# Performance work log

Hardware: AMD Instinct MI355X
Metric: run time of the kernel (lower is better)

The kernel has to match this reference:

```python
import jax, jax.numpy as jnp
import numpy as np

DEGREE = 4
NUM_CHARTS = 8
N = 16384
IN_DIM = 29  # 3*(2*4+1) + 2 procedural params


def positional_encoding(x, degree=DEGREE):
    # Faithful to torch order: [x, sin(2^1 pi x), cos(2^1 pi x), ..., sin(2^d pi x), cos(2^d pi x)]
    pe = [x]
    for d in range(1, degree + 1):
        s = (2.0 ** d) * np.pi
        pe.append(jnp.sin(s * x))
        pe.append(jnp.cos(s * x))
    return jnp.concatenate(pe, axis=-1)


def setup_inputs() -> dict:
    key = jax.random.key(0)
    ks = jax.random.split(key, 9)
    h = 256
    sc = 0.05
    return {
        "x": jax.random.normal(ks[0], (N, 3), jnp.float32),
        "proc": jax.random.normal(ks[1], (1, 2), jnp.float32),
        "W0": jax.random.normal(ks[2], (NUM_CHARTS, IN_DIM, h), jnp.float32) * sc,
        "b0": jax.random.normal(ks[3], (NUM_CHARTS, h), jnp.float32) * sc,
        "Wh": jax.random.normal(ks[4], (NUM_CHARTS, 6, h, h), jnp.float32) * sc,
        "bh": jax.random.normal(ks[5], (NUM_CHARTS, 6, h), jnp.float32) * sc,
        "Wl": jax.random.normal(ks[6], (NUM_CHARTS, h, 2), jnp.float32) * sc,
        "bl": jax.random.normal(ks[7], (NUM_CHARTS, 2), jnp.float32) * sc,
        "mlp_idx": jax.random.randint(ks[8], (N,), 0, NUM_CHARTS, jnp.int32),
    }


def reference(x, proc, W0, b0, Wh, bh, Wl, bl, mlp_idx):
    xp = positional_encoding(x)                      # (N, 27)
    proc_rep = jnp.broadcast_to(proc, (xp.shape[0], proc.shape[1]))
    xp = jnp.concatenate([xp, proc_rep], axis=-1)    # (N, 29)

    out = jnp.zeros((xp.shape[0], Wl.shape[-1]), xp.dtype)
    n_hidden = Wh.shape[1]
    for c in range(NUM_CHARTS):                      # small fixed chart loop
        h = jax.nn.relu(xp @ W0[c] + b0[c])          # (N, 256)
        for l in range(n_hidden):
            h = jax.nn.relu(h @ Wh[c, l] + bh[c, l])
        oc = jax.nn.sigmoid(h @ Wl[c] + bl[c])       # (N, 2)
        out = jnp.where((mlp_idx == c)[:, None], oc, out)
    return out
```

## Files before the change

kernel.cpp:

```cpp
#include <hip/hip_runtime.h>
#include <hip/hip_bf16.h>
#include <math.h>

#define NPTS   16384
#define NCH    8
#define MT     32
#define LSTR   264
#define SEG    16384
#define PSEG   2048

typedef short bf16x8 __attribute__((ext_vector_type(8)));
typedef float f32x4  __attribute__((ext_vector_type(4)));

__device__ __forceinline__ float bf2f(unsigned short u){
  union { unsigned int i; float f; } v; v.i = ((unsigned int)u) << 16; return v.f;
}
__device__ __forceinline__ unsigned short f2bf(float f){
  union { float f; unsigned int i; } v; v.f = f;
  unsigned int x = v.i;
  return (unsigned short)((x + 0x7fffu + ((x >> 16) & 1u)) >> 16);
}


__global__ __launch_bounds__(256) void prep_k(
    const float* __restrict__ Wh, const float* __restrict__ W0,
    const int* __restrict__ midx,
    unsigned short* __restrict__ Wth, unsigned short* __restrict__ Wt0,
    int* __restrict__ segcnt, int* __restrict__ bucket){
  int bid = blockIdx.x, tid = threadIdx.x;
  if (bid < 192){
    __shared__ __align__(16) unsigned short tile[64 * LSTR];
    int mat = bid >> 2, ck = bid & 3;
    const float* src = Wh + (size_t)mat * 65536 + (size_t)ck * 64 * 256;
    int r = tid >> 2, seg = (tid & 3) * 64;
    const float* sp = &src[r * 256 + seg];
    #pragma unroll
    for (int j8 = 0; j8 < 8; j8++){
      float4 f0 = *(const float4*)&sp[j8 * 8];
      float4 f1 = *(const float4*)&sp[j8 * 8 + 4];
      __align__(16) unsigned short t8[8];
      t8[0]=f2bf(f0.x); t8[1]=f2bf(f0.y); t8[2]=f2bf(f0.z); t8[3]=f2bf(f0.w);
      t8[4]=f2bf(f1.x); t8[5]=f2bf(f1.y); t8[6]=f2bf(f1.z); t8[7]=f2bf(f1.w);
      *(uint4*)&tile[r * LSTR + seg + j8 * 8] = *(const uint4*)t8;
    }
    __syncthreads();
    unsigned short* dst = Wth + (size_t)mat * 65536 + (size_t)ck * 16384;
    #pragma unroll
    for (int it = 0; it < 8; it++){
      int s = it * 256 + tid;
      int k8l = s >> 8, n = s & 255;
      __align__(16) unsigned short t8[8];
      #pragma unroll
      for (int j = 0; j < 8; j++) t8[j] = tile[(k8l * 8 + j) * LSTR + n];
      *(uint4*)&dst[(size_t)s * 8] = *(const uint4*)t8;
    }
  } else if (bid < 200){
    int c = bid - 192;
    #pragma unroll
    for (int it = 0; it < 4; it++){
      int s = it * 256 + tid;
      int k8 = s >> 8, n = s & 255;
      __align__(16) unsigned short t8[8];
      #pragma unroll
      for (int j = 0; j < 8; j++){
        int k = k8 * 8 + j;
        t8[j] = (k < 29) ? f2bf(W0[(c * 29 + k) * 256 + n]) : (unsigned short)0;
      }
      *(uint4*)&Wt0[(size_t)c * 8192 + (size_t)s * 8] = *(const uint4*)t8;
    }
  } else {
    __shared__ int cur[NCH];
    int sb = bid - 200;
    int lane = tid & 63;
    if (tid < NCH) cur[tid] = 0;
    __syncthreads();
    for (int it = 0; it < 8; it++){
      int i = sb * PSEG + it * 256 + tid;
      int c = midx[i];
      #pragma unroll
      for (int cc = 0; cc < NCH; cc++){
        unsigned long long m = __ballot(c == cc);
        if (!m) continue;
        int leader = (int)(__ffsll((long long)m) - 1);
        int wb = 0;
        if (lane == leader) wb = atomicAdd(&cur[cc], (int)__popcll(m));
        wb = __shfl(wb, leader);
        if (c == cc){
          int rk = (int)__popcll(m & ((1ull << lane) - 1));
          bucket[cc * SEG + sb * PSEG + wb + rk] = i;
        }
      }
    }
    __syncthreads();
    if (tid < NCH) segcnt[sb * NCH + tid] = cur[tid];
  }
}


__global__ __launch_bounds__(256) void mlp_k(
    const float* __restrict__ x,
    const float* __restrict__ proc,
    const float* __restrict__ b0,
    const float* __restrict__ bh,
    const float* __restrict__ Wl,
    const float* __restrict__ bl,
    const unsigned short* __restrict__ Wt0,
    const unsigned short* __restrict__ Wth,
    const int* __restrict__ segcnt,
    const int* __restrict__ bucket,
    float* __restrict__ out)
{
  __shared__ __align__(16) unsigned short actA[MT * LSTR];
  __shared__ __align__(16) unsigned short actB[MT * LSTR];
  __shared__ unsigned short biasb[7 * 256];
  __shared__ unsigned short wlb[512];
  __shared__ int ridx[MT];

  int chart = blockIdx.x & 7;
  int tile  = blockIdx.x >> 3;

  int pre[9];
  pre[0] = 0;
  #pragma unroll
  for (int s = 0; s < 8; s++) pre[s + 1] = pre[s] + segcnt[s * NCH + chart];
  int total = pre[8];
  int cnt = total - tile * MT;
  if (cnt <= 0) return;
  if (cnt > MT) cnt = MT;

  int tid  = threadIdx.x;
  int lane = tid & 63;
  int wv   = tid >> 6;
  int l15  = lane & 15;
  int quad = lane >> 4;
  int cb   = wv * 64;

  biasb[tid] = f2bf(b0[chart * 256 + tid]);
  #pragma unroll
  for (int j = 0; j < 6; j++)
    biasb[(j + 1) * 256 + tid] = f2bf(bh[(chart * 6 + j) * 256 + tid]);
  wlb[tid]       = f2bf(Wl[chart * 512 + tid]);
  wlb[256 + tid] = f2bf(Wl[chart * 512 + 256 + tid]);

  if (tid < MT){
    int row = tid;
    int g = -1;
    if (row < cnt){
      int r = tile * MT + row;
      int sb = 0, off = 0;
      #pragma unroll
      for (int s = 0; s < 8; s++)
        if (r >= pre[s]){ sb = s; off = r - pre[s]; }
      g = bucket[chart * SEG + sb * PSEG + off];
    }
    ridx[row] = g;
    unsigned short* rowp = &actA[row * LSTR];
    if (g >= 0){
      float xv0 = x[g*3+0], xv1 = x[g*3+1], xv2 = x[g*3+2];
      rowp[0] = f2bf(xv0); rowp[1] = f2bf(xv1); rowp[2] = f2bf(xv2);
      #pragma unroll
      for (int d = 1; d <= 4; d++){
        float s = (float)(1 << d) * 3.14159265358979323846f;
        int o = 3 + (d - 1) * 6;
        rowp[o+0] = f2bf(sinf(s*xv0)); rowp[o+1] = f2bf(sinf(s*xv1)); rowp[o+2] = f2bf(sinf(s*xv2));
        rowp[o+3] = f2bf(cosf(s*xv0)); rowp[o+4] = f2bf(cosf(s*xv1)); rowp[o+5] = f2bf(cosf(s*xv2));
      }
      rowp[27] = f2bf(proc[0]); rowp[28] = f2bf(proc[1]);
      rowp[29] = 0; rowp[30] = 0; rowp[31] = 0;
    } else {
      #pragma unroll
      for (int k = 0; k < 32; k++) rowp[k] = 0;
    }
  }
  __syncthreads();

  f32x4 acc[2][4];
  const f32x4 zz = {0.f, 0.f, 0.f, 0.f};

  {
    const unsigned short* W0p = Wt0 + chart * 8192;
    bf16x8 b0r[4];
    #pragma unroll
    for (int nt = 0; nt < 4; nt++)
      b0r[nt] = *(const bf16x8*)&W0p[(size_t)(quad * 256 + cb + nt * 16 + l15) * 8];
    #pragma unroll
    for (int mt = 0; mt < 2; mt++){
      bf16x8 a0 = *(const bf16x8*)&actA[(mt * 16 + l15) * LSTR + quad * 8];
      #pragma unroll
      for (int nt = 0; nt < 4; nt++)
        acc[mt][nt] = __builtin_amdgcn_mfma_f32_16x16x32_bf16(a0, b0r[nt], zz, 0, 0, 0);
    }
    #pragma unroll
    for (int nt = 0; nt < 4; nt++){
      int col = cb + nt * 16 + l15;
      float bias = bf2f(biasb[col]);
      #pragma unroll
      for (int mt = 0; mt < 2; mt++)
        #pragma unroll
        for (int r = 0; r < 4; r++){
          float v = acc[mt][nt][r] + bias;
          v = v > 0.f ? v : 0.f;
          actB[(mt * 16 + quad * 4 + r) * LSTR + col] = f2bf(v);
        }
    }
  }
  __syncthreads();

  for (int l = 1; l <= 6; l++){
    const unsigned short* wl8 = Wth + ((size_t)(chart * 6 + l - 1) << 16)
                              + (size_t)(cb + l15) * 8 + (size_t)quad * 2048;
    const unsigned short* ain = (l & 1) ? actB : actA;
    unsigned short* aout      = (l & 1) ? actA : actB;

    bf16x8 bcur[4], bnxt[4];
    #pragma unroll
    for (int nt = 0; nt < 4; nt++)
      bcur[nt] = *(const bf16x8*)&wl8[(size_t)nt * 128];

    #pragma unroll
    for (int kk = 0; kk < 8; kk++){
      if (kk < 7){
        const unsigned short* wn = wl8 + (size_t)(kk + 1) * 8192;
        #pragma unroll
        for (int nt = 0; nt < 4; nt++)
          bnxt[nt] = *(const bf16x8*)&wn[(size_t)nt * 128];
      }
      bf16x8 a0 = *(const bf16x8*)&ain[(0 * 16 + l15) * LSTR + kk * 32 + quad * 8];
      bf16x8 a1 = *(const bf16x8*)&ain[(1 * 16 + l15) * LSTR + kk * 32 + quad * 8];
      #pragma unroll
      for (int nt = 0; nt < 4; nt++){
        acc[0][nt] = __builtin_amdgcn_mfma_f32_16x16x32_bf16(
            a0, bcur[nt], (kk == 0) ? zz : acc[0][nt], 0, 0, 0);
        acc[1][nt] = __builtin_amdgcn_mfma_f32_16x16x32_bf16(
            a1, bcur[nt], (kk == 0) ? zz : acc[1][nt], 0, 0, 0);
      }
      #pragma unroll
      for (int nt = 0; nt < 4; nt++) bcur[nt] = bnxt[nt];
    }

    #pragma unroll
    for (int nt = 0; nt < 4; nt++){
      int col = cb + nt * 16 + l15;
      float bias = bf2f(biasb[l * 256 + col]);
      #pragma unroll
      for (int mt = 0; mt < 2; mt++)
        #pragma unroll
        for (int r = 0; r < 4; r++){
          float v = acc[mt][nt][r] + bias;
          v = v > 0.f ? v : 0.f;
          aout[(mt * 16 + quad * 4 + r) * LSTR + col] = f2bf(v);
        }
    }
    __syncthreads();
  }

  {
    int m = tid >> 3;
    int p = tid & 7;
    const unsigned short* hrow = actB + m * LSTR + p * 32;
    const unsigned short* wlp = wlb + p * 64;
    float s0 = 0.f, s1 = 0.f;
    #pragma unroll 8
    for (int k = 0; k < 32; k += 2){
      unsigned int w01 = *(const unsigned int*)&wlp[k * 2];
      unsigned int w23 = *(const unsigned int*)&wlp[k * 2 + 2];
      unsigned int h2  = *(const unsigned int*)&hrow[k];
      float hv0 = bf2f((unsigned short)(h2 & 0xffff));
      float hv1 = bf2f((unsigned short)(h2 >> 16));
      s0 += hv0 * bf2f((unsigned short)(w01 & 0xffff)) + hv1 * bf2f((unsigned short)(w23 & 0xffff));
      s1 += hv0 * bf2f((unsigned short)(w01 >> 16))    + hv1 * bf2f((unsigned short)(w23 >> 16));
    }
    s0 += __shfl_xor(s0, 1); s0 += __shfl_xor(s0, 2); s0 += __shfl_xor(s0, 4);
    s1 += __shfl_xor(s1, 1); s1 += __shfl_xor(s1, 2); s1 += __shfl_xor(s1, 4);
    if (p == 0){
      int g = ridx[m];
      if (g >= 0){
        float o0 = 1.f / (1.f + __expf(-(s0 + bl[chart*2+0])));
        float o1 = 1.f / (1.f + __expf(-(s1 + bl[chart*2+1])));
        *(float2*)&out[(size_t)g * 2] = make_float2(o0, o1);
      }
    }
  }
}


extern "C" void kernel_launch(void* const* d_in, const int* in_sizes, int n_in,
                              void* d_out, int out_size, void* d_ws, size_t ws_size,
                              hipStream_t stream){
  const float* x    = (const float*)d_in[0];
  const float* proc = (const float*)d_in[1];
  const float* W0   = (const float*)d_in[2];
  const float* b0   = (const float*)d_in[3];
  const float* Wh   = (const float*)d_in[4];
  const float* bh   = (const float*)d_in[5];
  const float* Wl   = (const float*)d_in[6];
  const float* bl   = (const float*)d_in[7];
  const int* midx = (const int*)d_in[8];
  float* out = (float*)d_out;

  char* ws = (char*)d_ws;
  int* segcnt = (int*)ws;
  int* bucket = segcnt + 64;
  size_t off = (((size_t)(64 + NCH * SEG)) * 4 + 15) & ~(size_t)15;
  unsigned short* Wt0 = (unsigned short*)(ws + off);
  unsigned short* Wth = Wt0 + NCH * 8192;

  hipLaunchKernelGGL(prep_k, dim3(208),  dim3(256), 0, stream,
                     Wh, W0, midx, Wth, Wt0, segcnt, bucket);
  hipLaunchKernelGGL(mlp_k,  dim3(4096), dim3(256), 0, stream,
                     x, proc, b0, bh, Wl, bl, Wt0, Wth, segcnt, bucket, out);
}
```

Before: 131.7 us.

## Issue all hidden-layer weight loads upfront with staged vmcnt waits

Replaces the double-buffered per-k-step weight prefetch in each hidden layer with inline asm that issues all 32 global dwordx4 loads at once. Explicit s_waitcnt vmcnt countdowns then let each k-group's MFMAs start as soon as that group's weights arrive. The aim is to expose more memory-level parallelism and keep the compiler from serializing the loads. The cost is 128 extra VGPRs of weight buffers per thread, which may reduce occupancy or cause spills. The hand-written vmcnt counts also make the code fragile if the compiler inserts other vector memory operations.

```diff
diff --git a/kernel.cpp b/kernel.cpp
--- a/kernel.cpp
+++ b/kernel.cpp
@@ -96,6 +96,33 @@
   }
 }
 
+
+#define LOADG(g) do {                                                          \
+    const unsigned short* _p = wlane + (size_t)(g) * 8192;                     \
+    asm volatile("global_load_dwordx4 %0, %4, off\n\t"                         \
+                 "global_load_dwordx4 %1, %4, off offset:256\n\t"              \
+                 "global_load_dwordx4 %2, %4, off offset:512\n\t"              \
+                 "global_load_dwordx4 %3, %4, off offset:768"                  \
+        : "=&v"(br[g][0]), "=&v"(br[g][1]), "=&v"(br[g][2]), "=&v"(br[g][3])   \
+        : "v"(_p));                                                            \
+  } while (0)
+
+#define WAITG(g, n)                                                            \
+  asm volatile("s_waitcnt vmcnt(" #n ")"                                       \
+      : "+v"(br[g][0]), "+v"(br[g][1]), "+v"(br[g][2]), "+v"(br[g][3]))
+
+#define MFMAG(g)                                                               \
+  {                                                                            \
+    bf16x8 a0 = *(const bf16x8*)&ain[(l15) * LSTR + (g) * 32 + quad * 8];      \
+    bf16x8 a1 = *(const bf16x8*)&ain[(16 + l15) * LSTR + (g) * 32 + quad * 8]; \
+    _Pragma("unroll")                                                          \
+    for (int nt = 0; nt < 4; nt++){                                            \
+      acc[0][nt] = __builtin_amdgcn_mfma_f32_16x16x32_bf16(                    \
+          a0, br[g][nt], ((g) == 0) ? zz : acc[0][nt], 0, 0, 0);               \
+      acc[1][nt] = __builtin_amdgcn_mfma_f32_16x16x32_bf16(                    \
+          a1, br[g][nt], ((g) == 0) ? zz : acc[1][nt], 0, 0, 0);               \
+    }                                                                          \
+  }
 
 __global__ __launch_bounds__(256) void mlp_k(
     const float* __restrict__ x,
@@ -207,36 +234,23 @@
   __syncthreads();
 
   for (int l = 1; l <= 6; l++){
-    const unsigned short* wl8 = Wth + ((size_t)(chart * 6 + l - 1) << 16)
-                              + (size_t)(cb + l15) * 8 + (size_t)quad * 2048;
+    const unsigned short* wlane = Wth + ((size_t)(chart * 6 + l - 1) << 16)
+                                + (size_t)(quad * 256 + cb + l15) * 8;
     const unsigned short* ain = (l & 1) ? actB : actA;
     unsigned short* aout      = (l & 1) ? actA : actB;
 
-    bf16x8 bcur[4], bnxt[4];
-    #pragma unroll
-    for (int nt = 0; nt < 4; nt++)
-      bcur[nt] = *(const bf16x8*)&wl8[(size_t)nt * 128];
-
-    #pragma unroll
-    for (int kk = 0; kk < 8; kk++){
-      if (kk < 7){
-        const unsigned short* wn = wl8 + (size_t)(kk + 1) * 8192;
-        #pragma unroll
-        for (int nt = 0; nt < 4; nt++)
-          bnxt[nt] = *(const bf16x8*)&wn[(size_t)nt * 128];
-      }
-      bf16x8 a0 = *(const bf16x8*)&ain[(0 * 16 + l15) * LSTR + kk * 32 + quad * 8];
-      bf16x8 a1 = *(const bf16x8*)&ain[(1 * 16 + l15) * LSTR + kk * 32 + quad * 8];
-      #pragma unroll
-      for (int nt = 0; nt < 4; nt++){
-        acc[0][nt] = __builtin_amdgcn_mfma_f32_16x16x32_bf16(
-            a0, bcur[nt], (kk == 0) ? zz : acc[0][nt], 0, 0, 0);
-        acc[1][nt] = __builtin_amdgcn_mfma_f32_16x16x32_bf16(
-            a1, bcur[nt], (kk == 0) ? zz : acc[1][nt], 0, 0, 0);
-      }
-      #pragma unroll
-      for (int nt = 0; nt < 4; nt++) bcur[nt] = bnxt[nt];
-    }
+    bf16x8 br[8][4];
+    LOADG(0); LOADG(1); LOADG(2); LOADG(3);
+    LOADG(4); LOADG(5); LOADG(6); LOADG(7);
+
+    WAITG(0, 28); MFMAG(0);
+    WAITG(1, 24); MFMAG(1);
+    WAITG(2, 20); MFMAG(2);
+    WAITG(3, 16); MFMAG(3);
+    WAITG(4, 12); MFMAG(4);
+    WAITG(5, 8);  MFMAG(5);
+    WAITG(6, 4);  MFMAG(6);
+    WAITG(7, 0);  MFMAG(7);
 
     #pragma unroll
     for (int nt = 0; nt < 4; nt++){
```

After: 128.6 us. 1.02x faster.
